# Performance work log

Hardware: AMD Instinct MI355X
Metric: run time of the kernel (lower is better)

Reference implementation:

```python
import jax, jax.numpy as jnp
import numpy as np

DIM = 1024
D_STATE = 64
D_CONV = 4
EXPAND = 2
N_HEADS = 8
D_INNER = DIM * EXPAND          # 2048
HEAD_DIM = D_INNER // N_HEADS   # 256
D_IN_PROJ = D_INNER + D_INNER + N_HEADS + D_STATE + D_STATE  # 4232
BATCH, SEQ = 2, 1024
EPS = 1e-6


def setup_inputs() -> dict:
    key = jax.random.key(0)
    ks = jax.random.split(key, 9)
    x = jax.random.normal(ks[0], (BATCH, SEQ, DIM), dtype=jnp.float32)
    in_proj_w = jax.random.normal(ks[1], (D_IN_PROJ, DIM), dtype=jnp.float32) * 0.02
    conv_w = jax.random.normal(ks[2], (D_INNER, D_CONV), dtype=jnp.float32) * 0.2
    conv_b = jax.random.normal(ks[3], (D_INNER,), dtype=jnp.float32) * 0.02
    A_log = jax.random.normal(ks[4], (N_HEADS,), dtype=jnp.float32) * 0.5
    D_param = jnp.ones((N_HEADS,), dtype=jnp.float32) + 0.1 * jax.random.normal(ks[5], (N_HEADS,), dtype=jnp.float32)
    dt_bias = jax.random.normal(ks[6], (N_HEADS,), dtype=jnp.float32) * 0.5
    norm_w = jnp.ones((D_INNER,), dtype=jnp.float32)
    out_proj_w = jax.random.normal(ks[7], (DIM, D_INNER), dtype=jnp.float32) * 0.02
    return {"x": x, "in_proj_w": in_proj_w, "conv_w": conv_w, "conv_b": conv_b,
            "A_log": A_log, "D_param": D_param, "dt_bias": dt_bias,
            "norm_w": norm_w, "out_proj_w": out_proj_w}


def _rms_norm(y, w):
    rms = jnp.sqrt(jnp.mean(y * y, axis=-1, keepdims=True) + EPS)
    return (y / rms) * w


def _depthwise_causal_conv(u, w, b):
    # u: (B, L, D_INNER); w: (D_INNER, D_CONV); torch Conv1d(pad=K-1)[..., :L]
    L = u.shape[1]
    up = jnp.pad(u, ((0, 0), (D_CONV - 1, 0), (0, 0)))
    out = b[None, None, :]
    for k in range(D_CONV):  # tiny fixed loop over taps
        out = out + up[:, k:k + L, :] * w[None, None, :, k]
    return out


def _mamba2_forward(x, in_proj_w, conv_w, conv_b, A_log, D_param, dt_bias, norm_w, out_proj_w):
    B_sz, L, _ = x.shape
    zxBCdt = x @ in_proj_w.T  # (B, L, D_IN_PROJ)
    z, xc, Bm, Cm, dt = jnp.split(
        zxBCdt, [D_INNER, 2 * D_INNER, 2 * D_INNER + N_HEADS, 2 * D_INNER + N_HEADS + D_STATE], axis=-1)
    # NOTE: split order matches torch .split([d_inner, d_inner, n_heads, d_state, d_state])
    xc = _depthwise_causal_conv(xc, conv_w, conv_b)
    xc = jax.nn.silu(xc)
    xh = xc.reshape(B_sz, L, N_HEADS, HEAD_DIM)  # (B, L, H, Dh)
    A = -jnp.exp(A_log)                          # (H,)
    dt = jax.nn.softplus(Bm + dt_bias)           # (B, L, H) -- torch split yields n_heads slice third
    a_bar = jnp.exp(dt * A[None, None, :])       # (B, L, H)

    # sequential SSD scan over L; carry h: (B, H, Dh, N)
    def step(h, t):
        a_t, b_t, c_t, x_t = t  # a:(B,H) b:(B,N) c:(B,N) x:(B,H,Dh)
        h = a_t[:, :, None, None] * h + b_t[:, None, None, :] * x_t[..., None]
        y_t = jnp.einsum('bhdn,bn->bhd', h, c_t)
        return h, y_t

    h0 = jnp.zeros((B_sz, N_HEADS, HEAD_DIM, D_STATE), dtype=x.dtype)
    xs = (jnp.moveaxis(a_bar, 1, 0), jnp.moveaxis(Cm, 1, 0) * 0 + jnp.moveaxis(Cm, 1, 0),
          jnp.moveaxis(dt, 1, 0) * 0, jnp.moveaxis(xh, 1, 0))  # placeholder, replaced below
    # Correct scan inputs: B proj = Cm slice? -- see split above: Bm is (B,L,H)? No:
    # split gives z:(..,D_INNER) xc:(..,D_INNER) third:(..,N_HEADS) fourth:(..,D_STATE) fifth:(..,D_STATE)
    # So dt-channels are the N_HEADS slice (Bm here), B is Cm, C is the last slice (dt var).
    B_proj, C_proj = Cm, dt if False else (Cm, None)
    raise NotImplementedError


def reference(x, in_proj_w, conv_w, conv_b, A_log, D_param, dt_bias, norm_w, out_proj_w):
    B_sz, L, _ = x.shape
    zxBCdt = x @ in_proj_w.T
    z = zxBCdt[..., :D_INNER]
    xc = zxBCdt[..., D_INNER:2 * D_INNER]
    Bp = zxBCdt[..., 2 * D_INNER:2 * D_INNER + N_HEADS]                      # torch 'B' slot? no:
    # torch split order: [d_inner, d_inner, n_heads, d_state, d_state] -> z, x, B, C, dt
    # so the n_heads-sized slice is named 'B' in torch code but used as B (input proj, size n_heads)?
    # In the torch code: z, x, B, C, dt = split([d_inner, d_inner, n_heads, d_state, d_state])
    # => B has size n_heads, C has size d_state, dt has size d_state. Faithfully reproduce that.
    Bm = zxBCdt[..., 2 * D_INNER:2 * D_INNER + N_HEADS]                       # (B,L,H)  -> 'B'
    Cm = zxBCdt[..., 2 * D_INNER + N_HEADS:2 * D_INNER + N_HEADS + D_STATE]   # (B,L,N)  -> 'C'
    dtm = zxBCdt[..., 2 * D_INNER + N_HEADS + D_STATE:]                       # (B,L,N)  -> 'dt'
    # ssd_scan(x, dt, A, B, C): dt broadcasts against dt_bias (H,) -> requires dt last dim == H.
    # The torch module passes dt of size d_state; with d_state=64 != n_heads this would error,
    # so faithful executable mapping uses the head-sized slice as dt and the two d_state slices as B, C.
    dt = jax.nn.softplus(Bm + dt_bias)            # (B, L, H)
    B_proj, C_proj = Cm, dtm                      # (B, L, N) each

    xc = _depthwise_causal_conv(xc, conv_w, conv_b)
    xc = jax.nn.silu(xc)
    xh = xc.reshape(B_sz, L, N_HEADS, HEAD_DIM)
    A = -jnp.exp(A_log)
    a_bar = jnp.exp(dt * A[None, None, :])        # (B, L, H)

    def step(h, t):
        a_t, b_t, c_t, x_t = t
        h = a_t[:, :, None, None] * h + b_t[:, None, None, :] * x_t[..., None]
        y_t = jnp.einsum('bhdn,bn->bhd', h, c_t)
        return h, y_t

    h0 = jnp.zeros((B_sz, N_HEADS, HEAD_DIM, D_STATE), dtype=x.dtype)
    ts = (jnp.moveaxis(a_bar, 1, 0), jnp.moveaxis(B_proj, 1, 0),
          jnp.moveaxis(C_proj, 1, 0), jnp.moveaxis(xh, 1, 0))
    _, ys = jax.lax.scan(step, h0, ts)
    y = jnp.moveaxis(ys, 0, 1)                    # (B, L, H, Dh)
    y = y + xh * D_param[None, None, :, None]
    y = y.reshape(B_sz, L, D_INNER)
    y = y * jax.nn.silu(z)
    y = _rms_norm(y, norm_w)
    return y @ out_proj_w.T
```

## Files before the change

### kernel.cpp

```cpp
#include <hip/hip_runtime.h>
#include <hip/hip_bf16.h>
#include <math.h>

#define DIM      1024
#define D_STATE  64
#define D_CONV   4
#define N_HEADS  8
#define D_INNER  2048
#define HEAD_DIM 256
#define NPROJ    4232
#define BATCH    2
#define SEQ      1024
#define M_ROWS   (BATCH * SEQ)
#define OFF_Z    0
#define OFF_XC   2048
#define OFF_DT   4096
#define OFF_B    4104
#define OFF_C    4168

#define CHUNK    64
#define N_CHUNK  (SEQ / CHUNK)
#define STATE_PER_BH (HEAD_DIM * D_STATE)

#define NPROJ_PAD 4352
#define PADT 72

typedef unsigned short u16;
typedef _Float16 f16x8 __attribute__((ext_vector_type(8)));
typedef float    f32x4 __attribute__((ext_vector_type(4)));

__device__ __forceinline__ u16 f2h(float f) {
    _Float16 h = (_Float16)f;
    return __builtin_bit_cast(u16, h);
}
__device__ __forceinline__ float h2f(u16 u) {
    return (float)__builtin_bit_cast(_Float16, u);
}

__device__ __forceinline__ void load_lds16(const void* g, void* l) {
    __builtin_amdgcn_global_load_lds((const __attribute__((address_space(1))) unsigned int*)g,
                                     (__attribute__((address_space(3))) unsigned int*)l,
                                     16, 0, 0);
}

__device__ __forceinline__ float softplus_f(float v) {
    return (v > 20.f) ? v : log1pf(expf(v));
}

__global__ __launch_bounds__(256) void cast2_kernel(
        const float* __restrict__ s0, u16* __restrict__ h0, int n0,
        const float* __restrict__ s1, u16* __restrict__ h1, int n1) {
    int i4 = (blockIdx.x * 256 + threadIdx.x) * 4;
    const float* src; u16* dst;
    if (i4 < n0) {
        src = s0; dst = h0;
    } else {
        i4 -= n0;
        if (i4 >= n1) return;
        src = s1; dst = h1;
    }
    float4 v = *(const float4*)&src[i4];
    ushort4 h;
    h.x = f2h(v.x); h.y = f2h(v.y); h.z = f2h(v.z); h.w = f2h(v.w);
    *(ushort4*)&dst[i4] = h;
}

__global__ __launch_bounds__(256) void cast_h_kernel(const float* __restrict__ src,
                                                     u16* __restrict__ hi, int n) {
    int i4 = (blockIdx.x * 256 + threadIdx.x) * 4;
    if (i4 >= n) return;
    float4 v = *(const float4*)&src[i4];
    ushort4 h;
    h.x = f2h(v.x); h.y = f2h(v.y); h.z = f2h(v.z); h.w = f2h(v.w);
    *(ushort4*)&hi[i4] = h;
}

template<int BN>
__global__ __launch_bounds__(256) void gemm_mfma1(const u16* __restrict__ Ah,
                                                  const u16* __restrict__ Bh,
                                                  float* __restrict__ C,
                                                  int K, int ldc, int Nstore,
                                                  int NrowsB, size_t zstride) {
    __shared__ u16 As[128 * 32];
    __shared__ u16 Bs[BN * 32];

    const int tid  = threadIdx.x;
    const int wave = tid >> 6;
    const int lane = tid & 63;
    const int fr   = lane & 15;
    const int kc   = lane >> 4;
    const int m0   = blockIdx.y * 128;
    const int n0   = blockIdx.x * BN;
    const int wm   = (wave & 1) * 64;
    const int wn   = (wave >> 1) * (BN / 2);

    const int kPer = K / gridDim.z;
    const int kBeg = blockIdx.z * kPer;
    C += (size_t)blockIdx.z * zstride;

    f32x4 acc[4][BN / 32];
#pragma unroll
    for (int i = 0; i < 4; ++i)
#pragma unroll
        for (int j = 0; j < BN / 32; ++j) acc[i][j] = (f32x4)0.f;

    for (int k0 = kBeg; k0 < kBeg + kPer; k0 += 32) {
        __syncthreads();
#pragma unroll
        for (int q = 0; q < 2; ++q) {
            int s = wave * 128 + q * 64 + lane;
            int r = s >> 2, pc = s & 3;
            int gc = pc ^ ((r >> 1) & 3);
            size_t goff = (size_t)(m0 + r) * K + k0 + gc * 8;
            load_lds16(Ah + goff, &As[(wave * 128 + q * 64) * 8]);
        }
#pragma unroll
        for (int q = 0; q < BN / 64; ++q) {
            int s = wave * BN + q * 64 + lane;
            int r = s >> 2, pc = s & 3;
            int gc = pc ^ ((r >> 1) & 3);
            if (n0 + r < NrowsB) {
                size_t goff = (size_t)(n0 + r) * K + k0 + gc * 8;
                load_lds16(Bh + goff, &Bs[(wave * BN + q * 64) * 8]);
            }
        }
        __syncthreads();

        f16x8 af[4];
#pragma unroll
        for (int i = 0; i < 4; ++i) {
            int r = wm + i * 16 + fr;
            int off = r * 32 + (kc ^ ((r >> 1) & 3)) * 8;
            af[i] = *(const f16x8*)&As[off];
        }
        f16x8 bf[BN / 32];
#pragma unroll
        for (int j = 0; j < BN / 32; ++j) {
            int r = wn + j * 16 + fr;
            int off = r * 32 + (kc ^ ((r >> 1) & 3)) * 8;
            bf[j] = *(const f16x8*)&Bs[off];
        }
#pragma unroll
        for (int i = 0; i < 4; ++i)
#pragma unroll
            for (int j = 0; j < BN / 32; ++j)
                acc[i][j] = __builtin_amdgcn_mfma_f32_16x16x32_f16(af[i], bf[j], acc[i][j], 0, 0, 0);
    }

    const int row0 = m0 + wm + (lane >> 4) * 4;
    const int colb = n0 + wn + fr;
#pragma unroll
    for (int i = 0; i < 4; ++i)
#pragma unroll
        for (int j = 0; j < BN / 32; ++j) {
            int col = colb + j * 16;
            if (col < Nstore) {
#pragma unroll
                for (int t = 0; t < 4; ++t)
                    C[(size_t)(row0 + i * 16 + t) * ldc + col] = acc[i][j][t];
            }
        }
}

__global__ __launch_bounds__(256) void reduce2_kernel(const float* __restrict__ p,
                                                      float* __restrict__ out, int n) {
    int i4 = (blockIdx.x * 256 + threadIdx.x) * 4;
    float4 a = *(const float4*)&p[i4];
    float4 b = *(const float4*)&p[(size_t)n + i4];
    *(float4*)&out[i4] = make_float4(a.x + b.x, a.y + b.y, a.z + b.z, a.w + b.w);
}

__global__ __launch_bounds__(256) void conv_silu_kernel(const float* __restrict__ zx,
                                                        const float* __restrict__ conv_w,
                                                        const float* __restrict__ conv_b,
                                                        const float* __restrict__ dt_bias,
                                                        const float* __restrict__ A_log,
                                                        u16* __restrict__ xh,
                                                        float* __restrict__ abar) {
    int idx = blockIdx.x * 256 + threadIdx.x;
    int c = idx & (D_INNER - 1);
    int m = idx >> 11;
    int l = m & (SEQ - 1);
    float acc = conv_b[c];
#pragma unroll
    for (int k = 0; k < D_CONV; ++k) {
        int lj = l + k - (D_CONV - 1);
        if (lj >= 0)
            acc = fmaf(zx[(size_t)(m + k - (D_CONV - 1)) * NPROJ + OFF_XC + c],
                       conv_w[c * D_CONV + k], acc);
    }
    xh[idx] = f2h(acc / (1.f + expf(-acc)));

    if (blockIdx.x < (M_ROWS * N_HEADS) / 256) {
        int di = blockIdx.x * 256 + threadIdx.x;
        int h = di & (N_HEADS - 1);
        int dm = di >> 3;
        float v = zx[(size_t)dm * NPROJ + OFF_DT + h] + dt_bias[h];
        abar[di] = expf(softplus_f(v) * -expf(A_log[h]));
    }
}

__global__ __launch_bounds__(256) void scan_local_mfma(const float* __restrict__ zx,
                                                       const u16* __restrict__ xh,
                                                       const float* __restrict__ dt_bias,
                                                       const float* __restrict__ A_log,
                                                       float* __restrict__ yscan,
                                                       float* __restrict__ Sloc) {
    const int blk = blockIdx.x;
    const int dq = blk & 3;
    const int c  = (blk >> 2) & (N_CHUNK - 1);
    const int bh = blk >> 6;
    const int hh = bh & (N_HEADS - 1);
    const int b  = bh >> 3;
    const int t    = threadIdx.x;
    const int wave = t >> 6;
    const int lane = t & 63;
    const int fr   = lane & 15;
    const int quad = lane >> 4;

    __shared__ float SDs[64];
    __shared__ u16 Ct [64 * PADT];
    __shared__ u16 Bt [64 * PADT];
    __shared__ u16 BwT[64 * PADT];
    __shared__ u16 Ps [64 * PADT];
    __shared__ u16 XsT[64 * PADT];

    const int m0   = b * SEQ + c * CHUNK;
    const int xcol = hh * HEAD_DIM + dq * 64;
    const float Ahd = -expf(A_log[hh]);
    const float dtb = dt_bias[hh];

    if (t < 64) {
        float d = softplus_f(zx[(size_t)(m0 + t) * NPROJ + OFF_DT + hh] + dtb);
#pragma unroll
        for (int off = 1; off < 64; off <<= 1) {
            float o = __shfl_up(d, off);
            if (lane >= off) d += o;
        }
        SDs[t] = d;
    }
    __syncthreads();
    const float SD63 = SDs[63];

#pragma unroll
    for (int i = 0; i < 16; ++i) {
        int idx = t + i * 256;
        int r = idx >> 6, n = idx & 63;
        size_t rowz = (size_t)(m0 + r) * NPROJ;
        float bv = zx[rowz + OFF_B + n];
        float cv = zx[rowz + OFF_C + n];
        Bt[r * PADT + n] = f2h(bv);
        Ct[r * PADT + n] = f2h(cv);
        float w2 = expf(Ahd * (SD63 - SDs[r]));
        BwT[n * PADT + r] = f2h(bv * w2);
        XsT[n * PADT + r] = xh[(size_t)(m0 + r) * D_INNER + xcol + n];
    }
    __syncthreads();

    const int tm0 = wave * 16;

    f32x4 g[4];
#pragma unroll
    for (int j = 0; j < 4; ++j) g[j] = (f32x4)0.f;
#pragma unroll
    for (int kk = 0; kk < 2; ++kk) {
        f16x8 af = *(const f16x8*)&Ct[(tm0 + fr) * PADT + kk * 32 + quad * 8];
#pragma unroll
        for (int j = 0; j < 4; ++j) {
            f16x8 bf = *(const f16x8*)&Bt[(j * 16 + fr) * PADT + kk * 32 + quad * 8];
            g[j] = __builtin_amdgcn_mfma_f32_16x16x32_f16(af, bf, g[j], 0, 0, 0);
        }
    }
    {
        int trow = tm0 + quad * 4;
#pragma unroll
        for (int j = 0; j < 4; ++j) {
#pragma unroll
            for (int reg = 0; reg < 4; ++reg) {
                int tt = trow + reg, ss = j * 16 + fr;
                float val = 0.f;
                if (ss <= tt) val = expf(Ahd * (SDs[tt] - SDs[ss])) * g[j][reg];
                Ps[tt * PADT + ss] = f2h(val);
            }
        }
    }

    f32x4 ya[4];
#pragma unroll
    for (int j = 0; j < 4; ++j) ya[j] = (f32x4)0.f;
#pragma unroll
    for (int kk = 0; kk < 2; ++kk) {
        f16x8 af = *(const f16x8*)&Ps[(tm0 + fr) * PADT + kk * 32 + quad * 8];
#pragma unroll
        for (int j = 0; j < 4; ++j) {
            f16x8 bf = *(const f16x8*)&XsT[(j * 16 + fr) * PADT + kk * 32 + quad * 8];
            ya[j] = __builtin_amdgcn_mfma_f32_16x16x32_f16(af, bf, ya[j], 0, 0, 0);
        }
    }
#pragma unroll
    for (int j = 0; j < 4; ++j)
#pragma unroll
        for (int reg = 0; reg < 4; ++reg) {
            int tt = tm0 + quad * 4 + reg;
            int dd = j * 16 + fr;
            yscan[(size_t)(m0 + tt) * D_INNER + xcol + dd] = ya[j][reg];
        }

    f32x4 sa[4];
#pragma unroll
    for (int j = 0; j < 4; ++j) sa[j] = (f32x4)0.f;
#pragma unroll
    for (int kk = 0; kk < 2; ++kk) {
        f16x8 af = *(const f16x8*)&BwT[(tm0 + fr) * PADT + kk * 32 + quad * 8];
#pragma unroll
        for (int j = 0; j < 4; ++j) {
            f16x8 bf = *(const f16x8*)&XsT[(j * 16 + fr) * PADT + kk * 32 + quad * 8];
            sa[j] = __builtin_amdgcn_mfma_f32_16x16x32_f16(af, bf, sa[j], 0, 0, 0);
        }
    }
    size_t sbase = (size_t)(bh * N_CHUNK + c) * STATE_PER_BH;
#pragma unroll
    for (int j = 0; j < 4; ++j)
#pragma unroll
        for (int reg = 0; reg < 4; ++reg) {
            int nn = tm0 + quad * 4 + reg;
            int dd = j * 16 + fr;
            Sloc[sbase + (size_t)nn * HEAD_DIM + dq * 64 + dd] = sa[j][reg];
        }
}

__global__ __launch_bounds__(256) void scan_combine_kernel(const float* __restrict__ abar,
                                                           float* __restrict__ Sloc) {
    const int blk = blockIdx.x;
    const int ds = blk & 15;
    const int bh = blk >> 4;
    const int hh = bh & (N_HEADS - 1);
    const int b  = bh >> 3;
    const int t  = threadIdx.x;

    __shared__ float PS[N_CHUNK];
    if (t < N_CHUNK) {
        float p = 1.f;
        int mbase = b * SEQ + t * CHUNK;
        for (int j = 0; j < CHUNK; ++j)
            p *= abar[(mbase + j) * N_HEADS + hh];
        PS[t] = p;
    }
    __syncthreads();

    float H[4] = {0.f, 0.f, 0.f, 0.f};
    for (int c = 0; c < N_CHUNK; ++c) {
        size_t base = (size_t)(bh * N_CHUNK + c) * STATE_PER_BH + ds * 1024 + t;
        float Sv[4];
#pragma unroll
        for (int i = 0; i < 4; ++i) Sv[i] = Sloc[base + i * 256];
#pragma unroll
        for (int i = 0; i < 4; ++i) Sloc[base + i * 256] = H[i];
        float P = PS[c];
#pragma unroll
        for (int i = 0; i < 4; ++i) H[i] = fmaf(P, H[i], Sv[i]);
    }
}

__global__ __launch_bounds__(256) void scan_corr_mfma(const float* __restrict__ zx,
                                                      const float* __restrict__ dt_bias,
                                                      const float* __restrict__ A_log,
                                                      const float* __restrict__ Hini,
                                                      float* __restrict__ yscan) {
    const int blk = blockIdx.x;
    const int dq = blk & 3;
    const int c  = (blk >> 2) & (N_CHUNK - 1);
    const int bh = blk >> 6;
    const int hh = bh & (N_HEADS - 1);
    const int b  = bh >> 3;
    const int t    = threadIdx.x;
    const int wave = t >> 6;
    const int lane = t & 63;
    const int fr   = lane & 15;
    const int quad = lane >> 4;

    __shared__ float SDs[64];
    __shared__ u16 Ct [64 * PADT];
    __shared__ u16 Hdn[64 * PADT];

    const int m0   = b * SEQ + c * CHUNK;
    const int xcol = hh * HEAD_DIM + dq * 64;
    const float Ahd = -expf(A_log[hh]);
    const float dtb = dt_bias[hh];

    if (t < 64) {
        float d = softplus_f(zx[(size_t)(m0 + t) * NPROJ + OFF_DT + hh] + dtb);
#pragma unroll
        for (int off = 1; off < 64; off <<= 1) {
            float o = __shfl_up(d, off);
            if (lane >= off) d += o;
        }
        SDs[t] = d;
    }

    size_t hbase = (size_t)(bh * N_CHUNK + c) * STATE_PER_BH;
#pragma unroll
    for (int i = 0; i < 16; ++i) {
        int idx = t + i * 256;
        int r = idx >> 6, n = idx & 63;
        Ct[r * PADT + n] = f2h(zx[(size_t)(m0 + r) * NPROJ + OFF_C + n]);
        Hdn[n * PADT + r] = f2h(Hini[hbase + (size_t)r * HEAD_DIM + dq * 64 + n]);
    }
    __syncthreads();

    const int tm0 = wave * 16;
    f32x4 ya[4];
#pragma unroll
    for (int j = 0; j < 4; ++j) ya[j] = (f32x4)0.f;
#pragma unroll
    for (int kk = 0; kk < 2; ++kk) {
        f16x8 af = *(const f16x8*)&Ct[(tm0 + fr) * PADT + kk * 32 + quad * 8];
#pragma unroll
        for (int j = 0; j < 4; ++j) {
            f16x8 bf = *(const f16x8*)&Hdn[(j * 16 + fr) * PADT + kk * 32 + quad * 8];
            ya[j] = __builtin_amdgcn_mfma_f32_16x16x32_f16(af, bf, ya[j], 0, 0, 0);
        }
    }
#pragma unroll
    for (int reg = 0; reg < 4; ++reg) {
        int tt = tm0 + quad * 4 + reg;
        float cum = expf(Ahd * SDs[tt]);
#pragma unroll
        for (int j = 0; j < 4; ++j) {
            int dd = j * 16 + fr;
            size_t off = (size_t)(m0 + tt) * D_INNER + xcol + dd;
            yscan[off] += cum * ya[j][reg];
        }
    }
}

__global__ __launch_bounds__(256) void gate_norm_kernel(const float* __restrict__ zx,
                                                        const u16* __restrict__ xh,
                                                        const float* __restrict__ Dp,
                                                        const float* __restrict__ nw,
                                                        const float* __restrict__ y,
                                                        u16* __restrict__ ybf_h) {
    const int m = blockIdx.x;
    const int t = threadIdx.x;
    const size_t rowz = (size_t)m * NPROJ;
    const size_t rowy = (size_t)m * D_INNER;

    float v[8];
    float ss = 0.f;
#pragma unroll
    for (int i = 0; i < 8; ++i) {
        int c = t + i * 256;
        float ys = fmaf(Dp[c >> 8], h2f(xh[rowy + c]), y[rowy + c]);
        float z  = zx[rowz + OFF_Z + c];
        float gated = ys * (z / (1.f + expf(-z)));
        v[i] = gated;
        ss += gated * gated;
    }
#pragma unroll
    for (int off = 1; off < 64; off <<= 1) ss += __shfl_xor(ss, off);

    __shared__ float red[4];
    if ((t & 63) == 0) red[t >> 6] = ss;
    __syncthreads();
    float tot = red[0] + red[1] + red[2] + red[3];
    float scale = 1.f / sqrtf(tot / (float)D_INNER + 1e-6f);

#pragma unroll
    for (int i = 0; i < 8; ++i) {
        int c = t + i * 256;
        float o = v[i] * scale * nw[c];
        ybf_h[rowy + c] = f2h(o);
    }
}

extern "C" void kernel_launch(void* const* d_in, const int* in_sizes, int n_in,
                              void* d_out, int out_size, void* d_ws, size_t ws_size,
                              hipStream_t stream) {
    const float* x         = (const float*)d_in[0];
    const float* in_proj_w = (const float*)d_in[1];
    const float* conv_w    = (const float*)d_in[2];
    const float* conv_b    = (const float*)d_in[3];
    const float* A_log     = (const float*)d_in[4];
    const float* D_param   = (const float*)d_in[5];
    const float* dt_bias   = (const float*)d_in[6];
    const float* norm_w    = (const float*)d_in[7];
    const float* out_proj_w= (const float*)d_in[8];
    float* out = (float*)d_out;

    float* ws  = (float*)d_ws;
    float* zx  = ws;
    float* R1  = zx + 8667136;
    float* R2  = R1 + 2166784;
    float* ab  = R2 + 4194304;
    float* R3  = ab + 16384;

    u16*  xh     = (u16*)R1;
    u16*  wobf_h = (u16*)R1;
    u16*  xbf_h  = (u16*)R2;
    float* ysc   = R2;
    u16*  wibf_h = (u16*)R3;
    float* Sloc  = R3;
    u16*  ybf_h  = (u16*)R3;
    float* pbuf  = zx;

    {
        int n0 = M_ROWS * DIM;
        int n1 = NPROJ * DIM;
        cast2_kernel<<<(n0 + n1) / 1024, 256, 0, stream>>>(
            x, xbf_h, n0, in_proj_w, wibf_h, n1);
    }

    gemm_mfma1<128><<<dim3(NPROJ_PAD / 128, M_ROWS / 128, 1), 256, 0, stream>>>(
        xbf_h, wibf_h, zx, DIM, NPROJ, NPROJ, NPROJ, 0);

    conv_silu_kernel<<<(M_ROWS * D_INNER) / 256, 256, 0, stream>>>(
        zx, conv_w, conv_b, dt_bias, A_log, xh, ab);

    scan_local_mfma<<<BATCH * N_HEADS * N_CHUNK * 4, 256, 0, stream>>>(
        zx, xh, dt_bias, A_log, ysc, Sloc);
    scan_combine_kernel<<<BATCH * N_HEADS * 16, 256, 0, stream>>>(ab, Sloc);
    scan_corr_mfma<<<BATCH * N_HEADS * N_CHUNK * 4, 256, 0, stream>>>(
        zx, dt_bias, A_log, Sloc, ysc);

    gate_norm_kernel<<<M_ROWS, 256, 0, stream>>>(
        zx, xh, D_param, norm_w, ysc, ybf_h);

    cast_h_kernel<<<(DIM * D_INNER) / 1024, 256, 0, stream>>>(
        out_proj_w, wobf_h, DIM * D_INNER);

    gemm_mfma1<64><<<dim3(DIM / 64, M_ROWS / 128, 2), 256, 0, stream>>>(
        ybf_h, wobf_h, pbuf, D_INNER, DIM, DIM, DIM,
        (size_t)M_ROWS * DIM);

    reduce2_kernel<<<(M_ROWS * DIM) / 1024, 256, 0, stream>>>(pbuf, out, M_ROWS * DIM);
}
```

Baseline: 224.8 us.

## Fuse intra-chunk output, gating and RMS stats into correction scan kernel

Moves the intra-chunk diagonal-block output computation from the first scan pass into the correction kernel. That kernel now also adds the D skip term, applies the SiLU(z) gate and writes fp16 y directly, while accumulating row sum-of-squares with atomics. The RMS scale moves to the final reduce kernel and norm_w is folded into the out_proj weight cast, which removes the gate_norm kernel and the fp32 yscan round trip. The chunk decay products now come from cumulative dt sums instead of a serial product over abar, so the abar computation in the conv kernel is dropped. In exchange it adds a memset and atomics, and normalisation is applied after the fp16 GEMM rather than before, which shifts precision slightly.

```diff
diff --git a/kernel.cpp b/kernel.cpp
--- a/kernel.cpp
+++ b/kernel.cpp
@@ -65,13 +65,18 @@
     *(ushort4*)&dst[i4] = h;
 }
 
-__global__ __launch_bounds__(256) void cast_h_kernel(const float* __restrict__ src,
-                                                     u16* __restrict__ hi, int n) {
+__global__ __launch_bounds__(256) void cast_hn_kernel(const float* __restrict__ src,
+                                                      const float* __restrict__ nw,
+                                                      u16* __restrict__ hi, int n) {
     int i4 = (blockIdx.x * 256 + threadIdx.x) * 4;
     if (i4 >= n) return;
     float4 v = *(const float4*)&src[i4];
+    int c = i4 & (D_INNER - 1);
     ushort4 h;
-    h.x = f2h(v.x); h.y = f2h(v.y); h.z = f2h(v.z); h.w = f2h(v.w);
+    h.x = f2h(v.x * nw[c]);
+    h.y = f2h(v.y * nw[c + 1]);
+    h.z = f2h(v.z * nw[c + 2]);
+    h.w = f2h(v.w * nw[c + 3]);
     *(ushort4*)&hi[i4] = h;
 }
 
@@ -162,21 +167,22 @@
         }
 }
 
-__global__ __launch_bounds__(256) void reduce2_kernel(const float* __restrict__ p,
-                                                      float* __restrict__ out, int n) {
+__global__ __launch_bounds__(256) void reduce2rms_kernel(const float* __restrict__ p,
+                                                         const float* __restrict__ rowSS,
+                                                         float* __restrict__ out, int n) {
     int i4 = (blockIdx.x * 256 + threadIdx.x) * 4;
+    int m = i4 >> 10;
+    float scale = rsqrtf(rowSS[m] * (1.f / (float)D_INNER) + 1e-6f);
     float4 a = *(const float4*)&p[i4];
     float4 b = *(const float4*)&p[(size_t)n + i4];
-    *(float4*)&out[i4] = make_float4(a.x + b.x, a.y + b.y, a.z + b.z, a.w + b.w);
+    *(float4*)&out[i4] = make_float4((a.x + b.x) * scale, (a.y + b.y) * scale,
+                                     (a.z + b.z) * scale, (a.w + b.w) * scale);
 }
 
 __global__ __launch_bounds__(256) void conv_silu_kernel(const float* __restrict__ zx,
                                                         const float* __restrict__ conv_w,
                                                         const float* __restrict__ conv_b,
-                                                        const float* __restrict__ dt_bias,
-                                                        const float* __restrict__ A_log,
-                                                        u16* __restrict__ xh,
-                                                        float* __restrict__ abar) {
+                                                        u16* __restrict__ xh) {
     int idx = blockIdx.x * 256 + threadIdx.x;
     int c = idx & (D_INNER - 1);
     int m = idx >> 11;
@@ -190,22 +196,14 @@
                        conv_w[c * D_CONV + k], acc);
     }
     xh[idx] = f2h(acc / (1.f + expf(-acc)));
-
-    if (blockIdx.x < (M_ROWS * N_HEADS) / 256) {
-        int di = blockIdx.x * 256 + threadIdx.x;
-        int h = di & (N_HEADS - 1);
-        int dm = di >> 3;
-        float v = zx[(size_t)dm * NPROJ + OFF_DT + h] + dt_bias[h];
-        abar[di] = expf(softplus_f(v) * -expf(A_log[h]));
-    }
-}
-
-__global__ __launch_bounds__(256) void scan_local_mfma(const float* __restrict__ zx,
+}
+
+__global__ __launch_bounds__(256) void scan_state_mfma(const float* __restrict__ zx,
                                                        const u16* __restrict__ xh,
                                                        const float* __restrict__ dt_bias,
                                                        const float* __restrict__ A_log,
-                                                       float* __restrict__ yscan,
-                                                       float* __restrict__ Sloc) {
+                                                       float* __restrict__ Sloc,
+                                                       float* __restrict__ csum) {
     const int blk = blockIdx.x;
     const int dq = blk & 3;
     const int c  = (blk >> 2) & (N_CHUNK - 1);
@@ -219,10 +217,7 @@
     const int quad = lane >> 4;
 
     __shared__ float SDs[64];
-    __shared__ u16 Ct [64 * PADT];
-    __shared__ u16 Bt [64 * PADT];
     __shared__ u16 BwT[64 * PADT];
-    __shared__ u16 Ps [64 * PADT];
     __shared__ u16 XsT[64 * PADT];
 
     const int m0   = b * SEQ + c * CHUNK;
@@ -241,16 +236,13 @@
     }
     __syncthreads();
     const float SD63 = SDs[63];
+    if (dq == 0 && t == 0) csum[bh * N_CHUNK + c] = SD63;
 
 #pragma unroll
     for (int i = 0; i < 16; ++i) {
         int idx = t + i * 256;
         int r = idx >> 6, n = idx & 63;
-        size_t rowz = (size_t)(m0 + r) * NPROJ;
-        float bv = zx[rowz + OFF_B + n];
-        float cv = zx[rowz + OFF_C + n];
-        Bt[r * PADT + n] = f2h(bv);
-        Ct[r * PADT + n] = f2h(cv);
+        float bv = zx[(size_t)(m0 + r) * NPROJ + OFF_B + n];
         float w2 = expf(Ahd * (SD63 - SDs[r]));
         BwT[n * PADT + r] = f2h(bv * w2);
         XsT[n * PADT + r] = xh[(size_t)(m0 + r) * D_INNER + xcol + n];
@@ -258,54 +250,6 @@
     __syncthreads();
 
     const int tm0 = wave * 16;
-
-    f32x4 g[4];
-#pragma unroll
-    for (int j = 0; j < 4; ++j) g[j] = (f32x4)0.f;
-#pragma unroll
-    for (int kk = 0; kk < 2; ++kk) {
-        f16x8 af = *(const f16x8*)&Ct[(tm0 + fr) * PADT + kk * 32 + quad * 8];
-#pragma unroll
-        for (int j = 0; j < 4; ++j) {
-            f16x8 bf = *(const f16x8*)&Bt[(j * 16 + fr) * PADT + kk * 32 + quad * 8];
-            g[j] = __builtin_amdgcn_mfma_f32_16x16x32_f16(af, bf, g[j], 0, 0, 0);
-        }
-    }
-    {
-        int trow = tm0 + quad * 4;
-#pragma unroll
-        for (int j = 0; j < 4; ++j) {
-#pragma unroll
-            for (int reg = 0; reg < 4; ++reg) {
-                int tt = trow + reg, ss = j * 16 + fr;
-                float val = 0.f;
-                if (ss <= tt) val = expf(Ahd * (SDs[tt] - SDs[ss])) * g[j][reg];
-                Ps[tt * PADT + ss] = f2h(val);
-            }
-        }
-    }
-
-    f32x4 ya[4];
-#pragma unroll
-    for (int j = 0; j < 4; ++j) ya[j] = (f32x4)0.f;
-#pragma unroll
-    for (int kk = 0; kk < 2; ++kk) {
-        f16x8 af = *(const f16x8*)&Ps[(tm0 + fr) * PADT + kk * 32 + quad * 8];
-#pragma unroll
-        for (int j = 0; j < 4; ++j) {
-            f16x8 bf = *(const f16x8*)&XsT[(j * 16 + fr) * PADT + kk * 32 + quad * 8];
-            ya[j] = __builtin_amdgcn_mfma_f32_16x16x32_f16(af, bf, ya[j], 0, 0, 0);
-        }
-    }
-#pragma unroll
-    for (int j = 0; j < 4; ++j)
-#pragma unroll
-        for (int reg = 0; reg < 4; ++reg) {
-            int tt = tm0 + quad * 4 + reg;
-            int dd = j * 16 + fr;
-            yscan[(size_t)(m0 + tt) * D_INNER + xcol + dd] = ya[j][reg];
-        }
-
     f32x4 sa[4];
 #pragma unroll
     for (int j = 0; j < 4; ++j) sa[j] = (f32x4)0.f;
@@ -329,44 +273,43 @@
         }
 }
 
-__global__ __launch_bounds__(256) void scan_combine_kernel(const float* __restrict__ abar,
-                                                           float* __restrict__ Sloc) {
+__global__ __launch_bounds__(256) void scan_combine2(const float* __restrict__ csum,
+                                                     const float* __restrict__ A_log,
+                                                     float* __restrict__ Sloc) {
     const int blk = blockIdx.x;
-    const int ds = blk & 15;
-    const int bh = blk >> 4;
-    const int hh = bh & (N_HEADS - 1);
-    const int b  = bh >> 3;
-    const int t  = threadIdx.x;
+    const int seg = blk & 63;
+    const int bh  = blk >> 6;
+    const int hh  = bh & (N_HEADS - 1);
+    const int t   = threadIdx.x;
 
     __shared__ float PS[N_CHUNK];
     if (t < N_CHUNK) {
-        float p = 1.f;
-        int mbase = b * SEQ + t * CHUNK;
-        for (int j = 0; j < CHUNK; ++j)
-            p *= abar[(mbase + j) * N_HEADS + hh];
-        PS[t] = p;
+        float Ahd = -expf(A_log[hh]);
+        PS[t] = expf(Ahd * csum[bh * N_CHUNK + t]);
     }
     __syncthreads();
 
-    float H[4] = {0.f, 0.f, 0.f, 0.f};
+    size_t base = (size_t)bh * N_CHUNK * STATE_PER_BH + seg * 256 + t;
+    float Sv[N_CHUNK];
+#pragma unroll
+    for (int c = 0; c < N_CHUNK; ++c)
+        Sv[c] = Sloc[base + (size_t)c * STATE_PER_BH];
+    float H = 0.f;
+#pragma unroll
     for (int c = 0; c < N_CHUNK; ++c) {
-        size_t base = (size_t)(bh * N_CHUNK + c) * STATE_PER_BH + ds * 1024 + t;
-        float Sv[4];
-#pragma unroll
-        for (int i = 0; i < 4; ++i) Sv[i] = Sloc[base + i * 256];
-#pragma unroll
-        for (int i = 0; i < 4; ++i) Sloc[base + i * 256] = H[i];
-        float P = PS[c];
-#pragma unroll
-        for (int i = 0; i < 4; ++i) H[i] = fmaf(P, H[i], Sv[i]);
-    }
-}
-
-__global__ __launch_bounds__(256) void scan_corr_mfma(const float* __restrict__ zx,
-                                                      const float* __restrict__ dt_bias,
-                                                      const float* __restrict__ A_log,
-                                                      const float* __restrict__ Hini,
-                                                      float* __restrict__ yscan) {
+        Sloc[base + (size_t)c * STATE_PER_BH] = H;
+        H = fmaf(PS[c], H, Sv[c]);
+    }
+}
+
+__global__ __launch_bounds__(256) void scan_ycorr_mfma(const float* __restrict__ zx,
+                                                       const u16* __restrict__ xh,
+                                                       const float* __restrict__ dt_bias,
+                                                       const float* __restrict__ A_log,
+                                                       const float* __restrict__ Dp,
+                                                       const float* __restrict__ Hini,
+                                                       u16* __restrict__ ybf,
+                                                       float* __restrict__ rowSS) {
     const int blk = blockIdx.x;
     const int dq = blk & 3;
     const int c  = (blk >> 2) & (N_CHUNK - 1);
@@ -381,6 +324,9 @@
 
     __shared__ float SDs[64];
     __shared__ u16 Ct [64 * PADT];
+    __shared__ u16 Bt [64 * PADT];
+    __shared__ u16 Ps [64 * PADT];
+    __shared__ u16 XsT[64 * PADT];
     __shared__ u16 Hdn[64 * PADT];
 
     const int m0   = b * SEQ + c * CHUNK;
@@ -397,79 +343,86 @@
         }
         SDs[t] = d;
     }
+    __syncthreads();
 
     size_t hbase = (size_t)(bh * N_CHUNK + c) * STATE_PER_BH;
 #pragma unroll
     for (int i = 0; i < 16; ++i) {
         int idx = t + i * 256;
         int r = idx >> 6, n = idx & 63;
-        Ct[r * PADT + n] = f2h(zx[(size_t)(m0 + r) * NPROJ + OFF_C + n]);
+        size_t rowz = (size_t)(m0 + r) * NPROJ;
+        Bt[r * PADT + n] = f2h(zx[rowz + OFF_B + n]);
+        Ct[r * PADT + n] = f2h(zx[rowz + OFF_C + n]);
+        XsT[n * PADT + r] = xh[(size_t)(m0 + r) * D_INNER + xcol + n];
         Hdn[n * PADT + r] = f2h(Hini[hbase + (size_t)r * HEAD_DIM + dq * 64 + n]);
     }
     __syncthreads();
 
     const int tm0 = wave * 16;
-    f32x4 ya[4];
-#pragma unroll
-    for (int j = 0; j < 4; ++j) ya[j] = (f32x4)0.f;
+
+    f32x4 g[4];
+#pragma unroll
+    for (int j = 0; j < 4; ++j) g[j] = (f32x4)0.f;
 #pragma unroll
     for (int kk = 0; kk < 2; ++kk) {
         f16x8 af = *(const f16x8*)&Ct[(tm0 + fr) * PADT + kk * 32 + quad * 8];
 #pragma unroll
         for (int j = 0; j < 4; ++j) {
-            f16x8 bf = *(const f16x8*)&Hdn[(j * 16 + fr) * PADT + kk * 32 + quad * 8];
-            ya[j] = __builtin_amdgcn_mfma_f32_16x16x32_f16(af, bf, ya[j], 0, 0, 0);
-        }
-    }
+            f16x8 bf = *(const f16x8*)&Bt[(j * 16 + fr) * PADT + kk * 32 + quad * 8];
+            g[j] = __builtin_amdgcn_mfma_f32_16x16x32_f16(af, bf, g[j], 0, 0, 0);
+        }
+    }
+    {
+        int trow = tm0 + quad * 4;
+#pragma unroll
+        for (int j = 0; j < 4; ++j) {
+#pragma unroll
+            for (int reg = 0; reg < 4; ++reg) {
+                int tt = trow + reg, ss = j * 16 + fr;
+                float val = 0.f;
+                if (ss <= tt) val = expf(Ahd * (SDs[tt] - SDs[ss])) * g[j][reg];
+                Ps[tt * PADT + ss] = f2h(val);
+            }
+        }
+    }
+
+    f32x4 ya[4], yb[4];
+#pragma unroll
+    for (int j = 0; j < 4; ++j) { ya[j] = (f32x4)0.f; yb[j] = (f32x4)0.f; }
+#pragma unroll
+    for (int kk = 0; kk < 2; ++kk) {
+        f16x8 afp = *(const f16x8*)&Ps[(tm0 + fr) * PADT + kk * 32 + quad * 8];
+        f16x8 afc = *(const f16x8*)&Ct[(tm0 + fr) * PADT + kk * 32 + quad * 8];
+#pragma unroll
+        for (int j = 0; j < 4; ++j) {
+            f16x8 bx = *(const f16x8*)&XsT[(j * 16 + fr) * PADT + kk * 32 + quad * 8];
+            f16x8 bh_ = *(const f16x8*)&Hdn[(j * 16 + fr) * PADT + kk * 32 + quad * 8];
+            ya[j] = __builtin_amdgcn_mfma_f32_16x16x32_f16(afp, bx, ya[j], 0, 0, 0);
+            yb[j] = __builtin_amdgcn_mfma_f32_16x16x32_f16(afc, bh_, yb[j], 0, 0, 0);
+        }
+    }
+
+    const float Dh = Dp[hh];
 #pragma unroll
     for (int reg = 0; reg < 4; ++reg) {
         int tt = tm0 + quad * 4 + reg;
         float cum = expf(Ahd * SDs[tt]);
+        size_t rowz = (size_t)(m0 + tt) * NPROJ;
+        size_t rowy = (size_t)(m0 + tt) * D_INNER + xcol;
+        float ss = 0.f;
 #pragma unroll
         for (int j = 0; j < 4; ++j) {
             int dd = j * 16 + fr;
-            size_t off = (size_t)(m0 + tt) * D_INNER + xcol + dd;
-            yscan[off] += cum * ya[j][reg];
-        }
-    }
-}
-
-__global__ __launch_bounds__(256) void gate_norm_kernel(const float* __restrict__ zx,
-                                                        const u16* __restrict__ xh,
-                                                        const float* __restrict__ Dp,
-                                                        const float* __restrict__ nw,
-                                                        const float* __restrict__ y,
-                                                        u16* __restrict__ ybf_h) {
-    const int m = blockIdx.x;
-    const int t = threadIdx.x;
-    const size_t rowz = (size_t)m * NPROJ;
-    const size_t rowy = (size_t)m * D_INNER;
-
-    float v[8];
-    float ss = 0.f;
-#pragma unroll
-    for (int i = 0; i < 8; ++i) {
-        int c = t + i * 256;
-        float ys = fmaf(Dp[c >> 8], h2f(xh[rowy + c]), y[rowy + c]);
-        float z  = zx[rowz + OFF_Z + c];
-        float gated = ys * (z / (1.f + expf(-z)));
-        v[i] = gated;
-        ss += gated * gated;
-    }
-#pragma unroll
-    for (int off = 1; off < 64; off <<= 1) ss += __shfl_xor(ss, off);
-
-    __shared__ float red[4];
-    if ((t & 63) == 0) red[t >> 6] = ss;
-    __syncthreads();
-    float tot = red[0] + red[1] + red[2] + red[3];
-    float scale = 1.f / sqrtf(tot / (float)D_INNER + 1e-6f);
-
-#pragma unroll
-    for (int i = 0; i < 8; ++i) {
-        int c = t + i * 256;
-        float o = v[i] * scale * nw[c];
-        ybf_h[rowy + c] = f2h(o);
+            float xv = h2f(XsT[dd * PADT + tt]);
+            float z  = zx[rowz + OFF_Z + xcol + dd];
+            float yv = ya[j][reg] + cum * yb[j][reg] + Dh * xv;
+            float gated = yv * (z / (1.f + expf(-z)));
+            ybf[rowy + dd] = f2h(gated);
+            ss += gated * gated;
+        }
+#pragma unroll
+        for (int off = 1; off < 16; off <<= 1) ss += __shfl_xor(ss, off);
+        if (fr == 0) atomicAdd(&rowSS[m0 + tt], ss);
     }
 }
 
@@ -497,12 +450,14 @@
     u16*  xh     = (u16*)R1;
     u16*  wobf_h = (u16*)R1;
     u16*  xbf_h  = (u16*)R2;
-    float* ysc   = R2;
+    u16*  ybf    = (u16*)R2;
+    float* csum  = ab;
+    float* rowSS = ab + 2048;
     u16*  wibf_h = (u16*)R3;
     float* Sloc  = R3;
-    u16*  ybf_h  = (u16*)R3;
     float* pbuf  = zx;
 
+    hipMemsetAsync(rowSS, 0, M_ROWS * sizeof(float), stream);
     {
         int n0 = M_ROWS * DIM;
         int n1 = NPROJ * DIM;
@@ -514,23 +469,21 @@
         xbf_h, wibf_h, zx, DIM, NPROJ, NPROJ, NPROJ, 0);
 
     conv_silu_kernel<<<(M_ROWS * D_INNER) / 256, 256, 0, stream>>>(
-        zx, conv_w, conv_b, dt_bias, A_log, xh, ab);
-
-    scan_local_mfma<<<BATCH * N_HEADS * N_CHUNK * 4, 256, 0, stream>>>(
-        zx, xh, dt_bias, A_log, ysc, Sloc);
-    scan_combine_kernel<<<BATCH * N_HEADS * 16, 256, 0, stream>>>(ab, Sloc);
-    scan_corr_mfma<<<BATCH * N_HEADS * N_CHUNK * 4, 256, 0, stream>>>(
-        zx, dt_bias, A_log, Sloc, ysc);
-
-    gate_norm_kernel<<<M_ROWS, 256, 0, stream>>>(
-        zx, xh, D_param, norm_w, ysc, ybf_h);
-
-    cast_h_kernel<<<(DIM * D_INNER) / 1024, 256, 0, stream>>>(
-        out_proj_w, wobf_h, DIM * D_INNER);
+        zx, conv_w, conv_b, xh);
+
+    scan_state_mfma<<<BATCH * N_HEADS * N_CHUNK * 4, 256, 0, stream>>>(
+        zx, xh, dt_bias, A_log, Sloc, csum);
+    scan_combine2<<<BATCH * N_HEADS * 64, 256, 0, stream>>>(csum, A_log, Sloc);
+    scan_ycorr_mfma<<<BATCH * N_HEADS * N_CHUNK * 4, 256, 0, stream>>>(
+        zx, xh, dt_bias, A_log, D_param, Sloc, ybf, rowSS);
+
+    cast_hn_kernel<<<(DIM * D_INNER) / 1024, 256, 0, stream>>>(
+        out_proj_w, norm_w, wobf_h, DIM * D_INNER);
 
     gemm_mfma1<64><<<dim3(DIM / 64, M_ROWS / 128, 2), 256, 0, stream>>>(
-        ybf_h, wobf_h, pbuf, D_INNER, DIM, DIM, DIM,
+        ybf, wobf_h, pbuf, D_INNER, DIM, DIM, DIM,
         (size_t)M_ROWS * DIM);
 
-    reduce2_kernel<<<(M_ROWS * DIM) / 1024, 256, 0, stream>>>(pbuf, out, M_ROWS * DIM);
-}
+    reduce2rms_kernel<<<(M_ROWS * DIM) / 1024, 256, 0, stream>>>(
+        pbuf, rowSS, out, M_ROWS * DIM);
+}
```

After: 205.0 us. 1.1x faster.
